# Kernel optimization log

Measured on AMD Instinct MI355X. Metric: run time of the kernel, lower is better.

Reference implementation:

```python
import jax, jax.numpy as jnp
import numpy as np

HORIZON = 8


def _gru_pass(seq, h0, w_ih, w_hh, b_ih, b_hh):
    """Run a single-layer PyTorch-convention GRU over seq (batch_first) starting
    from hidden h0; return the final hidden state (== out[:, -1, :]).
    seq: [B, T, I], h0: [B, H], w_ih: [3H, I], w_hh: [3H, H].
    Gate order (PyTorch): r, z, n."""
    # Precompute input projections for all timesteps: [B, T, 3H] -> [T, B, 3H]
    x_proj = jnp.einsum('bti,gi->btg', seq, w_ih) + b_ih
    x_proj = jnp.swapaxes(x_proj, 0, 1)

    def step(h, xp):
        hp = h @ w_hh.T + b_hh                      # [B, 3H]
        xr, xz, xn = jnp.split(xp, 3, axis=-1)
        hr, hz, hn = jnp.split(hp, 3, axis=-1)
        r = jax.nn.sigmoid(xr + hr)
        z = jax.nn.sigmoid(xz + hz)
        n = jnp.tanh(xn + r * hn)
        h_new = (1.0 - z) * n + z * h
        return h_new, None

    h_final, _ = jax.lax.scan(step, h0, x_proj)
    return h_final


def setup_inputs() -> dict:
    key = jax.random.key(0)
    ks = jax.random.split(key, 7)
    B, T, I, H = 256, 256, 64, 512
    scale = 0.04  # ~1/sqrt(H), matches PyTorch uniform init magnitude
    return {
        'x': jax.random.normal(ks[0], (B, T, I), dtype=jnp.float32),
        'w_ih': jax.random.normal(ks[1], (3 * H, I), dtype=jnp.float32) * scale,
        'w_hh': jax.random.normal(ks[2], (3 * H, H), dtype=jnp.float32) * scale,
        'b_ih': jax.random.normal(ks[3], (3 * H,), dtype=jnp.float32) * scale,
        'b_hh': jax.random.normal(ks[4], (3 * H,), dtype=jnp.float32) * scale,
        'fc_w': jax.random.normal(ks[5], (I, H), dtype=jnp.float32) * scale,
        'fc_b': jax.random.normal(ks[6], (I,), dtype=jnp.float32) * scale,
    }


def reference(x, w_ih, w_hh, b_ih, b_hh, fc_w, fc_b):
    """Faithful translation of PredictorRNN.forward: each horizon step re-runs
    the GRU over the whole growing sequence, carrying hidden state h between
    passes (matching the original torch code's out,h = rnn(seq, h))."""
    B = x.shape[0]
    H = w_hh.shape[1]
    h = jnp.zeros((B, H), dtype=x.dtype)  # h=None -> zeros in torch
    seq = x
    preds = []
    for _ in range(HORIZON):
        h = _gru_pass(seq, h, w_ih, w_hh, b_ih, b_hh)  # == out[:, -1, :]
        step = h @ fc_w.T + fc_b                       # [B, I]
        preds.append(step)
        seq = jnp.concatenate([seq, step[:, None, :]], axis=1)
    return jnp.stack(preds, axis=1)  # [B, horizon, I]
```

## Files before the change

### kernel.cpp

```cpp
#include <hip/hip_runtime.h>


typedef __attribute__((ext_vector_type(8))) short short8;
typedef __attribute__((ext_vector_type(4))) float floatx4;

#define B_    256
#define T_    256
#define I_    64
#define H_    512
#define HZ    8
#define LPAD  520
#define HLSZ  (16 * LPAD)

#define MFMA_BF16(acc, a, b) \
  acc = __builtin_amdgcn_mfma_f32_16x16x32_bf16((a), (b), (acc), 0, 0, 0)

#define POLL_BACKOFF(it)                         \
  do {                                           \
    if ((it) < 2)      __builtin_amdgcn_s_sleep(1);  \
    else if ((it) < 8) __builtin_amdgcn_s_sleep(4);  \
    else               __builtin_amdgcn_s_sleep(16); \
  } while (0)
#define POLL_TIGHT(it)                           \
  do {                                           \
    if ((it) < 4)       __builtin_amdgcn_s_sleep(1); \
    else if ((it) < 16) __builtin_amdgcn_s_sleep(2); \
    else                __builtin_amdgcn_s_sleep(8); \
  } while (0)

__device__ __forceinline__ float bf2f(unsigned short u) {
  union { unsigned int i; float f; } v; v.i = ((unsigned int)u) << 16; return v.f;
}
__device__ __forceinline__ unsigned short f2bf(float f) {
  union { float f; unsigned int i; } v; v.f = f;
  return (unsigned short)((v.i + 0x7FFFu + ((v.i >> 16) & 1u)) >> 16);
}
__device__ __forceinline__ short8 ld8_f32_to_bf16(const float* p) {
  short8 r;
#pragma unroll
  for (int e = 0; e < 8; ++e) r[e] = (short)f2bf(p[e]);
  return r;
}
__device__ __forceinline__ float sigm(float xx) {
  return __builtin_amdgcn_rcpf(1.f + __expf(-xx));
}
__device__ __forceinline__ float tanh_fast(float xx) {
  float e = __expf(2.f * xx);
  return 1.f - 2.f * __builtin_amdgcn_rcpf(e + 1.f);
}
__device__ __forceinline__ unsigned long long ald64(const unsigned int* p) {
  return __hip_atomic_load((const unsigned long long*)p, __ATOMIC_RELAXED,
                           __HIP_MEMORY_SCOPE_AGENT);
}
__device__ __forceinline__ void ast32(unsigned int* p, unsigned int v) {
  __hip_atomic_store(p, v, __ATOMIC_RELAXED, __HIP_MEMORY_SCOPE_AGENT);
}

__device__ __forceinline__ void stage_h16(unsigned short* hl,
                                          const unsigned int* hb,
                                          unsigned int want, int tid) {
  unsigned long long v[16];
#pragma unroll
  for (int i = 0; i < 16; ++i)
    v[i] = ald64(hb + (size_t)i * H_ + 2 * tid);
  int it = 0;
  for (;;) {
    bool all = true, ok15 = true;
#pragma unroll
    for (int i = 0; i < 16; ++i) {
      unsigned int w0 = (unsigned int)v[i];
      unsigned int w1 = (unsigned int)(v[i] >> 32);
      if (((w0 >> 16) != want) || ((w1 >> 16) != want)) {
        all = false;
        if (i == 15) ok15 = false;
      }
    }
    if (all) break;
    if (!ok15) {
      POLL_TIGHT(it); ++it;
      v[15] = ald64(hb + (size_t)15 * H_ + 2 * tid);
    } else {
#pragma unroll
      for (int i = 0; i < 15; ++i) {
        unsigned int w0 = (unsigned int)v[i];
        unsigned int w1 = (unsigned int)(v[i] >> 32);
        if (((w0 >> 16) != want) || ((w1 >> 16) != want))
          v[i] = ald64(hb + (size_t)i * H_ + 2 * tid);
      }
      __builtin_amdgcn_s_sleep(1);
    }
  }
#pragma unroll
  for (int i = 0; i < 16; ++i) {
    unsigned int w0 = (unsigned int)v[i];
    unsigned int w1 = (unsigned int)(v[i] >> 32);
    *(unsigned int*)&hl[i * LPAD + 2 * tid] = (w0 & 0xffffu) | (w1 << 16);
  }
}

extern "C" __global__ void __launch_bounds__(256, 1)
gru_chain(const float* __restrict__ x,
          const float* __restrict__ w_ih,
          const float* __restrict__ w_hh,
          const float* __restrict__ b_ih,
          const float* __restrict__ b_hh,
          const float* __restrict__ fc_w,
          const float* __restrict__ fc_b,
          float* __restrict__ out,
          unsigned int* __restrict__ hbuf,
          unsigned int* __restrict__ xext)
{
  const int tid  = threadIdx.x;
  const int wave = tid >> 6;
  const int lane = tid & 63;
  const int bx   = blockIdx.x;
  const int grp  = bx & 15;
  const int ju   = ((bx >> 4) << 2) | wave;
  const int n16  = lane & 15;
  const int quad = lane >> 4;
  const int jg   = ju * 16 + n16;
  const int rowbase = grp * 16;

  __shared__ __align__(16) unsigned short hls[2 * HLSZ];

  short8 wR[18], wZ[18], wHN[16], wXN[2];
  {
    const int koff = quad * 8;
    const float* whr = w_hh + (size_t)(0 * H_ + jg) * H_ + koff;
    const float* whz = w_hh + (size_t)(1 * H_ + jg) * H_ + koff;
    const float* whn = w_hh + (size_t)(2 * H_ + jg) * H_ + koff;
#pragma unroll
    for (int kc = 0; kc < 16; ++kc) {
      wR[kc]  = ld8_f32_to_bf16(whr + kc * 32);
      wZ[kc]  = ld8_f32_to_bf16(whz + kc * 32);
      wHN[kc] = ld8_f32_to_bf16(whn + kc * 32);
    }
    const float* wir = w_ih + (size_t)(0 * H_ + jg) * I_ + koff;
    const float* wiz = w_ih + (size_t)(1 * H_ + jg) * I_ + koff;
    const float* win = w_ih + (size_t)(2 * H_ + jg) * I_ + koff;
#pragma unroll
    for (int kc = 0; kc < 2; ++kc) {
      wR[16 + kc] = ld8_f32_to_bf16(wir + kc * 32);
      wZ[16 + kc] = ld8_f32_to_bf16(wiz + kc * 32);
      wXN[kc]     = ld8_f32_to_bf16(win + kc * 32);
    }
  }
  const float brc = b_ih[jg]          + b_hh[jg];
  const float bzc = b_ih[H_ + jg]     + b_hh[H_ + jg];
  const float bxn = b_ih[2 * H_ + jg];
  const float bhn = b_hh[2 * H_ + jg];

  float hloc[4] = {0.f, 0.f, 0.f, 0.f};

  int s = 0;
  for (int p = 0; p < HZ; ++p) {
    const int Tp = T_ + p;
    for (int t = 0; t < Tp; ++t) {
      short8 xaf0, xaf1;
      if (t < T_) {
        const float* xs = x + ((size_t)(rowbase + n16) * T_ + t) * I_ + quad * 8;
        xaf0 = ld8_f32_to_bf16(xs);
        xaf1 = ld8_f32_to_bf16(xs + 32);
      }
      unsigned short* hl = &hls[(s & 1) * HLSZ];
      if (s > 0) {
        const unsigned int* hb = hbuf + (size_t)((s + 1) & 1) * (B_ * H_) +
                                 (size_t)rowbase * H_;
        stage_h16(hl, hb, (unsigned int)s, tid);
      } else {
#pragma unroll
        for (int i = 0; i < 16; ++i)
          *(unsigned int*)&hl[i * LPAD + 2 * tid] = 0u;
      }
      if (t >= T_) {
        const int p2 = t - T_;
        const unsigned int wantx = (unsigned int)(p2 + 1);
        const unsigned int* xb =
            xext + ((size_t)p2 * B_ + rowbase + n16) * I_;
        unsigned long long u[8];
#pragma unroll
        for (int k = 0; k < 8; ++k) {
          int off = (k < 4) ? (quad * 8 + 2 * k) : (32 + quad * 8 + 2 * (k - 4));
          u[k] = ald64(xb + off);
        }
        int it = 0;
        for (;;) {
          bool all = true;
#pragma unroll
          for (int k = 0; k < 8; ++k) {
            unsigned int w0 = (unsigned int)u[k];
            unsigned int w1 = (unsigned int)(u[k] >> 32);
            if (((w0 >> 16) != wantx) || ((w1 >> 16) != wantx)) {
              all = false;
              int off = (k < 4) ? (quad * 8 + 2 * k)
                                : (32 + quad * 8 + 2 * (k - 4));
              u[k] = ald64(xb + off);
            }
          }
          if (all) break;
          POLL_BACKOFF(it);
          ++it;
        }
#pragma unroll
        for (int k = 0; k < 4; ++k) {
          xaf0[2 * k]     = (short)(unsigned short)u[k];
          xaf0[2 * k + 1] = (short)(unsigned short)(u[k] >> 32);
          xaf1[2 * k]     = (short)(unsigned short)u[4 + k];
          xaf1[2 * k + 1] = (short)(unsigned short)(u[4 + k] >> 32);
        }
      }
      __syncthreads();
      short8 haf[16];
#pragma unroll
      for (int kc = 0; kc < 16; ++kc)
        haf[kc] = *(const short8*)&hl[n16 * LPAD + kc * 32 + quad * 8];

      floatx4 aR = {0.f, 0.f, 0.f, 0.f};
      floatx4 aZ = {0.f, 0.f, 0.f, 0.f};
      floatx4 aN = {0.f, 0.f, 0.f, 0.f};
      floatx4 aX = {0.f, 0.f, 0.f, 0.f};
#pragma unroll
      for (int kc = 0; kc < 16; ++kc) {
        MFMA_BF16(aR, haf[kc], wR[kc]);
        MFMA_BF16(aZ, haf[kc], wZ[kc]);
        MFMA_BF16(aN, haf[kc], wHN[kc]);
      }
      MFMA_BF16(aR, xaf0, wR[16]);  MFMA_BF16(aR, xaf1, wR[17]);
      MFMA_BF16(aZ, xaf0, wZ[16]);  MFMA_BF16(aZ, xaf1, wZ[17]);
      MFMA_BF16(aX, xaf0, wXN[0]);  MFMA_BF16(aX, xaf1, wXN[1]);

      unsigned int* hd = hbuf + (size_t)(s & 1) * (B_ * H_);
      const unsigned int tg = ((unsigned int)(s + 1)) << 16;
#pragma unroll
      for (int i = 0; i < 4; ++i) {
        float rv = sigm(aR[i] + brc);
        float zv = sigm(aZ[i] + bzc);
        float nv = tanh_fast(aX[i] + bxn + rv * (aN[i] + bhn));
        float hn = (1.f - zv) * nv + zv * hloc[i];
        hloc[i]  = hn;
        ast32(&hd[(size_t)(rowbase + quad * 4 + i) * H_ + jg],
              tg | (unsigned int)f2bf(hn));
      }
      ++s;
    }
    {
      unsigned short* hl = &hls[(s & 1) * HLSZ];
      const unsigned int* hb = hbuf + (size_t)((s + 1) & 1) * (B_ * H_) +
                               (size_t)rowbase * H_;
      stage_h16(hl, hb, (unsigned int)s, tid);
      __syncthreads();
      const int mm  = lane & 15;
      const int sub = lane >> 4;
#pragma unroll
      for (int cc = 0; cc < 2; ++cc) {
        const int c = ju * 2 + cc;
        const unsigned short* hrow = &hl[mm * LPAD + sub * 128];
        const float* wrow = fc_w + (size_t)c * H_ + sub * 128;
        float acc = 0.f;
#pragma unroll
        for (int kk = 0; kk < 128; kk += 8) {
          short8 hv = *(const short8*)(hrow + kk);
#pragma unroll
          for (int e = 0; e < 8; ++e)
            acc = fmaf(bf2f((unsigned short)hv[e]), wrow[kk + e], acc);
        }
        acc += __shfl_xor(acc, 16, 64);
        acc += __shfl_xor(acc, 32, 64);
        if (sub == 0) {
          float val = acc + fc_b[c];
          out[((size_t)(rowbase + mm) * HZ + p) * I_ + c] = val;
          ast32(&xext[((size_t)p * B_ + rowbase + mm) * I_ + c],
                (((unsigned int)(p + 1)) << 16) | (unsigned int)f2bf(val));
        }
      }
      __syncthreads();
    }
  }
}

extern "C" void kernel_launch(void* const* d_in, const int* in_sizes, int n_in,
                              void* d_out, int out_size, void* d_ws, size_t ws_size,
                              hipStream_t stream) {
  const float* x    = (const float*)d_in[0];
  const float* w_ih = (const float*)d_in[1];
  const float* w_hh = (const float*)d_in[2];
  const float* b_ih = (const float*)d_in[3];
  const float* b_hh = (const float*)d_in[4];
  const float* fc_w = (const float*)d_in[5];
  const float* fc_b = (const float*)d_in[6];
  float* out = (float*)d_out;

  unsigned char* ws = (unsigned char*)d_ws;
  const size_t hbuf_b = (size_t)2 * B_ * H_ * 4;
  const size_t xext_b = (size_t)HZ * B_ * I_ * 4;
  unsigned int* hbuf = (unsigned int*)ws;
  unsigned int* xext = (unsigned int*)(ws + hbuf_b);

  hipMemsetAsync(d_ws, 0, hbuf_b + xext_b, stream);

  gru_chain<<<dim3(128), dim3(256), 0, stream>>>(
      x, w_ih, w_hh, b_ih, b_hh, fc_w, fc_b, out, hbuf, xext);
}
```

Before: 6.416 ms.

## Replace per-element tagged hidden-state polling with per-wave flags and packed bf16 exchange

Result: slower. 10.99 ms (+71.3%).

```diff
diff --git a/kernel.cpp b/kernel.cpp
--- a/kernel.cpp
+++ b/kernel.cpp
@@ -11,6 +11,8 @@
 #define HZ    8
 #define LPAD  520
 #define HLSZ  (16 * LPAD)
+#define HPAIR (H_ / 2)
+#define HSLAB (B_ * HPAIR)
 
 #define MFMA_BF16(acc, a, b) \
   acc = __builtin_amdgcn_mfma_f32_16x16x32_bf16((a), (b), (acc), 0, 0, 0)
@@ -21,12 +23,6 @@
     else if ((it) < 8) __builtin_amdgcn_s_sleep(4);  \
     else               __builtin_amdgcn_s_sleep(16); \
   } while (0)
-#define POLL_TIGHT(it)                           \
-  do {                                           \
-    if ((it) < 4)       __builtin_amdgcn_s_sleep(1); \
-    else if ((it) < 16) __builtin_amdgcn_s_sleep(2); \
-    else                __builtin_amdgcn_s_sleep(8); \
-  } while (0)
 
 __device__ __forceinline__ float bf2f(unsigned short u) {
   union { unsigned int i; float f; } v; v.i = ((unsigned int)u) << 16; return v.f;
@@ -56,45 +52,31 @@
   __hip_atomic_store(p, v, __ATOMIC_RELAXED, __HIP_MEMORY_SCOPE_AGENT);
 }
 
-__device__ __forceinline__ void stage_h16(unsigned short* hl,
-                                          const unsigned int* hb,
-                                          unsigned int want, int tid) {
-  unsigned long long v[16];
-#pragma unroll
-  for (int i = 0; i < 16; ++i)
-    v[i] = ald64(hb + (size_t)i * H_ + 2 * tid);
-  int it = 0;
-  for (;;) {
-    bool all = true, ok15 = true;
-#pragma unroll
-    for (int i = 0; i < 16; ++i) {
-      unsigned int w0 = (unsigned int)v[i];
-      unsigned int w1 = (unsigned int)(v[i] >> 32);
-      if (((w0 >> 16) != want) || ((w1 >> 16) != want)) {
-        all = false;
-        if (i == 15) ok15 = false;
-      }
-    }
-    if (all) break;
-    if (!ok15) {
-      POLL_TIGHT(it); ++it;
-      v[15] = ald64(hb + (size_t)15 * H_ + 2 * tid);
-    } else {
-#pragma unroll
-      for (int i = 0; i < 15; ++i) {
-        unsigned int w0 = (unsigned int)v[i];
-        unsigned int w1 = (unsigned int)(v[i] >> 32);
-        if (((w0 >> 16) != want) || ((w1 >> 16) != want))
-          v[i] = ald64(hb + (size_t)i * H_ + 2 * tid);
-      }
-      __builtin_amdgcn_s_sleep(1);
-    }
+__device__ __forceinline__ void stage_h_flags(unsigned short* hl,
+                                              const unsigned int* hb,
+                                              const unsigned int* fl,
+                                              unsigned int want,
+                                              int tid, int lane) {
+  unsigned int f = want;
+  if (lane < 32)
+    f = __hip_atomic_load(&fl[lane], __ATOMIC_ACQUIRE,
+                          __HIP_MEMORY_SCOPE_AGENT);
+  while (!__all((int)(f >= want))) {
+    __builtin_amdgcn_s_sleep(1);
+    if (lane < 32)
+      f = __hip_atomic_load(&fl[lane], __ATOMIC_ACQUIRE,
+                            __HIP_MEMORY_SCOPE_AGENT);
   }
-#pragma unroll
-  for (int i = 0; i < 16; ++i) {
-    unsigned int w0 = (unsigned int)v[i];
-    unsigned int w1 = (unsigned int)(v[i] >> 32);
-    *(unsigned int*)&hl[i * LPAD + 2 * tid] = (w0 & 0xffffu) | (w1 << 16);
+  __builtin_amdgcn_sched_barrier(0);
+  unsigned long long v[8];
+#pragma unroll
+  for (int k = 0; k < 8; ++k)
+    v[k] = ald64(hb + (((size_t)k * 256 + tid) << 1));
+#pragma unroll
+  for (int k = 0; k < 8; ++k) {
+    const int r  = 2 * k + (tid >> 7);
+    const int cu = (2 * tid) & 255;
+    *(unsigned long long*)&hl[r * LPAD + cu * 2] = v[k];
   }
 }
 
@@ -108,20 +90,25 @@
           const float* __restrict__ fc_b,
           float* __restrict__ out,
           unsigned int* __restrict__ hbuf,
-          unsigned int* __restrict__ xext)
+          unsigned int* __restrict__ xext,
+          unsigned int* __restrict__ flags)
 {
   const int tid  = threadIdx.x;
   const int wave = tid >> 6;
   const int lane = tid & 63;
   const int bx   = blockIdx.x;
   const int grp  = bx & 15;
-  const int ju   = ((bx >> 4) << 2) | wave;
+  const int blk  = bx >> 4;
+  const int ju   = (blk << 2) | wave;
   const int n16  = lane & 15;
   const int quad = lane >> 4;
   const int jg   = ju * 16 + n16;
   const int rowbase = grp * 16;
 
   __shared__ __align__(16) unsigned short hls[2 * HLSZ];
+
+  unsigned int* gfl = flags + grp * 64;
+  const int     fidx = blk * 4 + wave;
 
   short8 wR[18], wZ[18], wHN[16], wXN[2];
   {
@@ -164,13 +151,16 @@
       }
       unsigned short* hl = &hls[(s & 1) * HLSZ];
       if (s > 0) {
-        const unsigned int* hb = hbuf + (size_t)((s + 1) & 1) * (B_ * H_) +
-                                 (size_t)rowbase * H_;
-        stage_h16(hl, hb, (unsigned int)s, tid);
+        const unsigned int* hb = hbuf + (size_t)((s + 1) & 1) * HSLAB +
+                                 (size_t)rowbase * HPAIR;
+        stage_h_flags(hl, hb, gfl, (unsigned int)s, tid, lane);
       } else {
 #pragma unroll
-        for (int i = 0; i < 16; ++i)
-          *(unsigned int*)&hl[i * LPAD + 2 * tid] = 0u;
+        for (int k = 0; k < 8; ++k) {
+          const int r  = 2 * k + (tid >> 7);
+          const int cu = (2 * tid) & 255;
+          *(unsigned long long*)&hl[r * LPAD + cu * 2] = 0ull;
+        }
       }
       if (t >= T_) {
         const int p2 = t - T_;
@@ -229,8 +219,9 @@
       MFMA_BF16(aZ, xaf0, wZ[16]);  MFMA_BF16(aZ, xaf1, wZ[17]);
       MFMA_BF16(aX, xaf0, wXN[0]);  MFMA_BF16(aX, xaf1, wXN[1]);
 
-      unsigned int* hd = hbuf + (size_t)(s & 1) * (B_ * H_);
-      const unsigned int tg = ((unsigned int)(s + 1)) << 16;
+      unsigned int* hd = hbuf + (size_t)(s & 1) * HSLAB +
+                         (size_t)rowbase * HPAIR;
+      unsigned int bs[4];
 #pragma unroll
       for (int i = 0; i < 4; ++i) {
         float rv = sigm(aR[i] + brc);
@@ -238,16 +229,35 @@
         float nv = tanh_fast(aX[i] + bxn + rv * (aN[i] + bhn));
         float hn = (1.f - zv) * nv + zv * hloc[i];
         hloc[i]  = hn;
-        ast32(&hd[(size_t)(rowbase + quad * 4 + i) * H_ + jg],
-              tg | (unsigned int)f2bf(hn));
+        bs[i]    = (unsigned int)f2bf(hn);
+      }
+      {
+        unsigned int p01 = bs[0] | (bs[1] << 16);
+        unsigned int p23 = bs[2] | (bs[3] << 16);
+        unsigned int q01 = __shfl_xor(p01, 1, 64);
+        unsigned int q23 = __shfl_xor(p23, 1, 64);
+        const int cp = ju * 8 + (n16 >> 1);
+        if ((n16 & 1) == 0) {
+          ast32(&hd[(size_t)(quad * 4 + 0) * HPAIR + cp],
+                (p01 & 0xFFFFu) | (q01 << 16));
+          ast32(&hd[(size_t)(quad * 4 + 1) * HPAIR + cp],
+                (p01 >> 16) | (q01 & 0xFFFF0000u));
+        } else {
+          ast32(&hd[(size_t)(quad * 4 + 2) * HPAIR + cp],
+                (q23 & 0xFFFFu) | (p23 << 16));
+          ast32(&hd[(size_t)(quad * 4 + 3) * HPAIR + cp],
+                (q23 >> 16) | (p23 & 0xFFFF0000u));
+        }
+        asm volatile("s_waitcnt vmcnt(0)" ::: "memory");
+        if (lane == 0) ast32(&gfl[fidx], (unsigned int)(s + 1));
       }
       ++s;
     }
     {
       unsigned short* hl = &hls[(s & 1) * HLSZ];
-      const unsigned int* hb = hbuf + (size_t)((s + 1) & 1) * (B_ * H_) +
-                               (size_t)rowbase * H_;
-      stage_h16(hl, hb, (unsigned int)s, tid);
+      const unsigned int* hb = hbuf + (size_t)((s + 1) & 1) * HSLAB +
+                               (size_t)rowbase * HPAIR;
+      stage_h_flags(hl, hb, gfl, (unsigned int)s, tid, lane);
       __syncthreads();
       const int mm  = lane & 15;
       const int sub = lane >> 4;
@@ -291,13 +301,15 @@
   float* out = (float*)d_out;
 
   unsigned char* ws = (unsigned char*)d_ws;
-  const size_t hbuf_b = (size_t)2 * B_ * H_ * 4;
-  const size_t xext_b = (size_t)HZ * B_ * I_ * 4;
-  unsigned int* hbuf = (unsigned int*)ws;
-  unsigned int* xext = (unsigned int*)(ws + hbuf_b);
-
-  hipMemsetAsync(d_ws, 0, hbuf_b + xext_b, stream);
+  const size_t hbuf_b  = (size_t)2 * HSLAB * 4;
+  const size_t xext_b  = (size_t)HZ * B_ * I_ * 4;
+  const size_t flags_b = (size_t)16 * 64 * 4;
+  unsigned int* hbuf  = (unsigned int*)ws;
+  unsigned int* xext  = (unsigned int*)(ws + hbuf_b);
+  unsigned int* flags = (unsigned int*)(ws + hbuf_b + xext_b);
+
+  hipMemsetAsync(d_ws, 0, hbuf_b + xext_b + flags_b, stream);
 
   gru_chain<<<dim3(128), dim3(256), 0, stream>>>(
-      x, w_ih, w_hh, b_ih, b_hh, fc_w, fc_b, out, hbuf, xext);
-}
+      x, w_ih, w_hh, b_ih, b_hh, fc_w, fc_b, out, hbuf, xext, flags);
+}
```
